# Kernel optimization log

Measured on AMD Instinct MI355X. Metric: run time of the kernel, lower is better.

Reference implementation:

```python
import jax, jax.numpy as jnp
import numpy as np

N = 16384
T = 100          # num_timesteps
THR = 1.0        # spike threshold
TAU = 10.0       # tau_mem
WIDTH = 1.0      # surrogate beta (width_grad)
SCALE = 1.0      # surrogate grad scale (scale_grad)
ALPHA = float(np.exp(-1.0 / TAU))  # membrane decay per step


@jax.custom_vjp
def single_spike(v):
    # SingleSpike: at most one spike per step, heaviside on (v - thr)
    return (v >= THR).astype(v.dtype)

def _ss_fwd(v):
    return single_spike(v), v

def _ss_bwd(v, g):
    # SingleExponential surrogate: scale * exp(-beta * |v - thr|)
    return (g * SCALE * jnp.exp(-WIDTH * jnp.abs(v - THR)),)

single_spike.defvjp(_ss_fwd, _ss_bwd)


def setup_inputs() -> dict:
    key = jax.random.key(0)
    k1, k2 = jax.random.split(key)
    x = jax.random.normal(k1, (N, 2, 4, 4, T), dtype=jnp.float32)
    # SLAYER dense weight: Conv3d kernel [out=1, C=2, H=4, W=4] (no bias)
    W = jax.random.normal(k2, (1, 2, 4, 4), dtype=jnp.float32) * 0.1
    return {"x": x, "W": W}


def reference(x, W):
    # dense projection per timestep: [N,C,H,W,T] x [O,C,H,W] -> [N,O,T]
    weighted = jnp.einsum('nchwt,ochw->not', x, W)
    inp_t = jnp.moveaxis(weighted, -1, 0)  # [T, N, 1]

    def step(v, i):
        # sinabs LIF with norm_input=True: v = alpha*v + (1-alpha)*input
        v = ALPHA * v + (1.0 - ALPHA) * i
        s = single_spike(v)
        return v - s * THR, s  # MembraneSubtract reset

    v0 = jnp.zeros(inp_t.shape[1:], dtype=weighted.dtype)
    _, spikes = jax.lax.scan(step, v0, inp_t)  # spikes: [T, N, 1]
    out = jnp.moveaxis(spikes, 0, -1)          # [N, 1, T]
    return out.reshape(x.shape[0], 1, 1, 1, T)  # match Conv3d output shape
```

## Files before the change

### kernel.cpp

```cpp
#include <hip/hip_runtime.h>


#define T_STEPS 100
#define CHW     32
#define NPB     16
#define PITCH   101

__global__ __launch_bounds__(256, 4)
void exodus_fused(const float* __restrict__ x,
                  const float* __restrict__ W,
                  float* __restrict__ out) {
    __shared__ float s_in[NPB][PITCH];
    __shared__ float s_sp[NPB][PITCH];

    const int tid    = threadIdx.x;
    const int lane   = tid & 63;
    const int wv     = tid >> 6;
    const int n_base = blockIdx.x * NPB;

    float Wr[CHW];
    #pragma unroll
    for (int c = 0; c < CHW; ++c) Wr[c] = W[c];

    if (lane < T_STEPS / 2) {
        for (int i = 0; i < NPB / 4; ++i) {
            const int nl = wv * (NPB / 4) + i;
            const float* xp = x + (size_t)(n_base + nl) * (CHW * T_STEPS) + 2 * lane;
            float a0 = 0.f, a1 = 0.f;
            #pragma unroll
            for (int c = 0; c < CHW; ++c) {
                const float2 v = *reinterpret_cast<const float2*>(xp + c * T_STEPS);
                a0 += Wr[c] * v.x;
                a1 += Wr[c] * v.y;
            }
            s_in[nl][2 * lane]     = a0;
            s_in[nl][2 * lane + 1] = a1;
        }
    }
    __syncthreads();

    if (lane < NPB / 4) {
        const int nl = wv * (NPB / 4) + lane;
        const float A = 0.9048374180359595f;
        const float B = 0.0951625819640404f;
        float v = 0.f;
        #pragma unroll 4
        for (int t = 0; t < T_STEPS; ++t) {
            v = A * v + B * s_in[nl][t];
            const float sp = (v >= 1.0f) ? 1.0f : 0.0f;
            v -= sp;
            s_sp[nl][t] = sp;
        }
    }
    __syncthreads();

    float* op = out + (size_t)n_base * T_STEPS;
    for (int k = tid; k < NPB * T_STEPS; k += 256) {
        op[k] = s_sp[k / T_STEPS][k % T_STEPS];
    }
}

extern "C" void kernel_launch(void* const* d_in, const int* in_sizes, int n_in,
                              void* d_out, int out_size, void* d_ws, size_t ws_size,
                              hipStream_t stream) {
    const float* x = (const float*)d_in[0];
    const float* W = (const float*)d_in[1];
    float* out = (float*)d_out;

    const int N = in_sizes[0] / (CHW * T_STEPS);
    const int grid = N / NPB;
    exodus_fused<<<grid, 256, 0, stream>>>(x, W, out);
}
```

Measured before the change: 38.66 us.

## Halve neurons per block and software-pipeline x loads with double register buffers

```diff
diff --git a/kernel.cpp b/kernel.cpp
--- a/kernel.cpp
+++ b/kernel.cpp
@@ -3,7 +3,8 @@
 
 #define T_STEPS 100
 #define CHW     32
-#define NPB     16
+#define NPW     2
+#define NPB     8
 #define PITCH   101
 
 __global__ __launch_bounds__(256, 4)
@@ -23,30 +24,62 @@
     for (int c = 0; c < CHW; ++c) Wr[c] = W[c];
 
     if (lane < T_STEPS / 2) {
-        for (int i = 0; i < NPB / 4; ++i) {
-            const int nl = wv * (NPB / 4) + i;
-            const float* xp = x + (size_t)(n_base + nl) * (CHW * T_STEPS) + 2 * lane;
-            float a0 = 0.f, a1 = 0.f;
-            #pragma unroll
-            for (int c = 0; c < CHW; ++c) {
-                const float2 v = *reinterpret_cast<const float2*>(xp + c * T_STEPS);
-                a0 += Wr[c] * v.x;
-                a1 += Wr[c] * v.y;
-            }
-            s_in[nl][2 * lane]     = a0;
-            s_in[nl][2 * lane + 1] = a1;
+        const float* xw = x + (size_t)(n_base + wv * NPW) * (CHW * T_STEPS) + 2 * lane;
+        const int NSTR = CHW * T_STEPS;
+
+        float2 bA[16], bB[16];
+        #pragma unroll
+        for (int j = 0; j < 16; ++j)
+            bA[j] = *reinterpret_cast<const float2*>(xw + j * T_STEPS);
+        #pragma unroll
+        for (int j = 0; j < 16; ++j)
+            bB[j] = *reinterpret_cast<const float2*>(xw + (16 + j) * T_STEPS);
+
+        float n0x = 0.f, n0y = 0.f;
+        #pragma unroll
+        for (int j = 0; j < 16; ++j) {
+            n0x = fmaf(Wr[j], bA[j].x, n0x);
+            n0y = fmaf(Wr[j], bA[j].y, n0y);
         }
+        #pragma unroll
+        for (int j = 0; j < 16; ++j)
+            bA[j] = *reinterpret_cast<const float2*>(xw + NSTR + j * T_STEPS);
+        #pragma unroll
+        for (int j = 0; j < 16; ++j) {
+            n0x = fmaf(Wr[16 + j], bB[j].x, n0x);
+            n0y = fmaf(Wr[16 + j], bB[j].y, n0y);
+        }
+        s_in[wv * NPW + 0][2 * lane]     = n0x;
+        s_in[wv * NPW + 0][2 * lane + 1] = n0y;
+
+        #pragma unroll
+        for (int j = 0; j < 16; ++j)
+            bB[j] = *reinterpret_cast<const float2*>(xw + NSTR + (16 + j) * T_STEPS);
+
+        float n1x = 0.f, n1y = 0.f;
+        #pragma unroll
+        for (int j = 0; j < 16; ++j) {
+            n1x = fmaf(Wr[j], bA[j].x, n1x);
+            n1y = fmaf(Wr[j], bA[j].y, n1y);
+        }
+        #pragma unroll
+        for (int j = 0; j < 16; ++j) {
+            n1x = fmaf(Wr[16 + j], bB[j].x, n1x);
+            n1y = fmaf(Wr[16 + j], bB[j].y, n1y);
+        }
+        s_in[wv * NPW + 1][2 * lane]     = n1x;
+        s_in[wv * NPW + 1][2 * lane + 1] = n1y;
     }
     __syncthreads();
 
-    if (lane < NPB / 4) {
-        const int nl = wv * (NPB / 4) + lane;
+    if (lane < NPW) {
+        const int nl = wv * NPW + lane;
         const float A = 0.9048374180359595f;
         const float B = 0.0951625819640404f;
         float v = 0.f;
         #pragma unroll 4
         for (int t = 0; t < T_STEPS; ++t) {
-            v = A * v + B * s_in[nl][t];
+            v = fmaf(A, v, B * s_in[nl][t]);
             const float sp = (v >= 1.0f) ? 1.0f : 0.0f;
             v -= sp;
             s_sp[nl][t] = sp;
```

After: 37.28 us (median of 2 runs). -3.6%, faster.

## Use float4 loads with explicit double-buffering and halve neurons per block

Applied to the files above, without the earlier changes.

```diff
diff --git a/kernel.cpp b/kernel.cpp
--- a/kernel.cpp
+++ b/kernel.cpp
@@ -3,8 +3,9 @@
 
 #define T_STEPS 100
 #define CHW     32
-#define NPB     16
-#define PITCH   101
+#define NPW     2
+#define NPB     8
+#define PITCH   104
 
 __global__ __launch_bounds__(256, 4)
 void exodus_fused(const float* __restrict__ x,
@@ -22,31 +23,69 @@
     #pragma unroll
     for (int c = 0; c < CHW; ++c) Wr[c] = W[c];
 
-    if (lane < T_STEPS / 2) {
-        for (int i = 0; i < NPB / 4; ++i) {
-            const int nl = wv * (NPB / 4) + i;
-            const float* xp = x + (size_t)(n_base + nl) * (CHW * T_STEPS) + 2 * lane;
-            float a0 = 0.f, a1 = 0.f;
-            #pragma unroll
-            for (int c = 0; c < CHW; ++c) {
-                const float2 v = *reinterpret_cast<const float2*>(xp + c * T_STEPS);
-                a0 += Wr[c] * v.x;
-                a1 += Wr[c] * v.y;
-            }
-            s_in[nl][2 * lane]     = a0;
-            s_in[nl][2 * lane + 1] = a1;
+    if (lane < 50) {
+        const int nl = lane / 25;
+        const int qd = lane - nl * 25;
+        const float* xp = x + (size_t)(n_base + wv * NPW + nl) * (CHW * T_STEPS)
+                        + qd * 4;
+
+        float4 bA[8], bB[8];
+        float4 acc = {0.f, 0.f, 0.f, 0.f};
+
+        #pragma unroll
+        for (int j = 0; j < 8; ++j)
+            bA[j] = *reinterpret_cast<const float4*>(xp + j * T_STEPS);
+        #pragma unroll
+        for (int j = 0; j < 8; ++j)
+            bB[j] = *reinterpret_cast<const float4*>(xp + (8 + j) * T_STEPS);
+
+        #pragma unroll
+        for (int j = 0; j < 8; ++j) {
+            acc.x = fmaf(Wr[j], bA[j].x, acc.x);
+            acc.y = fmaf(Wr[j], bA[j].y, acc.y);
+            acc.z = fmaf(Wr[j], bA[j].z, acc.z);
+            acc.w = fmaf(Wr[j], bA[j].w, acc.w);
         }
+        #pragma unroll
+        for (int j = 0; j < 8; ++j)
+            bA[j] = *reinterpret_cast<const float4*>(xp + (16 + j) * T_STEPS);
+        #pragma unroll
+        for (int j = 0; j < 8; ++j) {
+            acc.x = fmaf(Wr[8 + j], bB[j].x, acc.x);
+            acc.y = fmaf(Wr[8 + j], bB[j].y, acc.y);
+            acc.z = fmaf(Wr[8 + j], bB[j].z, acc.z);
+            acc.w = fmaf(Wr[8 + j], bB[j].w, acc.w);
+        }
+        #pragma unroll
+        for (int j = 0; j < 8; ++j)
+            bB[j] = *reinterpret_cast<const float4*>(xp + (24 + j) * T_STEPS);
+        #pragma unroll
+        for (int j = 0; j < 8; ++j) {
+            acc.x = fmaf(Wr[16 + j], bA[j].x, acc.x);
+            acc.y = fmaf(Wr[16 + j], bA[j].y, acc.y);
+            acc.z = fmaf(Wr[16 + j], bA[j].z, acc.z);
+            acc.w = fmaf(Wr[16 + j], bA[j].w, acc.w);
+        }
+        #pragma unroll
+        for (int j = 0; j < 8; ++j) {
+            acc.x = fmaf(Wr[24 + j], bB[j].x, acc.x);
+            acc.y = fmaf(Wr[24 + j], bB[j].y, acc.y);
+            acc.z = fmaf(Wr[24 + j], bB[j].z, acc.z);
+            acc.w = fmaf(Wr[24 + j], bB[j].w, acc.w);
+        }
+
+        *reinterpret_cast<float4*>(&s_in[wv * NPW + nl][qd * 4]) = acc;
     }
     __syncthreads();
 
-    if (lane < NPB / 4) {
-        const int nl = wv * (NPB / 4) + lane;
+    if (lane < NPW) {
+        const int nl = wv * NPW + lane;
         const float A = 0.9048374180359595f;
         const float B = 0.0951625819640404f;
         float v = 0.f;
         #pragma unroll 4
         for (int t = 0; t < T_STEPS; ++t) {
-            v = A * v + B * s_in[nl][t];
+            v = fmaf(A, v, B * s_in[nl][t]);
             const float sp = (v >= 1.0f) ? 1.0f : 0.0f;
             v -= sp;
             s_sp[nl][t] = sp;
@@ -54,9 +93,12 @@
     }
     __syncthreads();
 
-    float* op = out + (size_t)n_base * T_STEPS;
-    for (int k = tid; k < NPB * T_STEPS; k += 256) {
-        op[k] = s_sp[k / T_STEPS][k % T_STEPS];
+    if (tid < NPB * T_STEPS / 4) {
+        const int t4 = tid * 4;
+        const int n  = t4 / T_STEPS;
+        const int t  = t4 - n * T_STEPS;
+        *reinterpret_cast<float4*>(out + (size_t)n_base * T_STEPS + t4) =
+            *reinterpret_cast<const float4*>(&s_sp[n][t]);
     }
 }
 
```

Result: no change. 38.11 us (-1.4%).

## Make each wave independent with register double-buffered loads overlapping the scan

Applied to the files above, without the earlier changes.

```diff
diff --git a/kernel.cpp b/kernel.cpp
--- a/kernel.cpp
+++ b/kernel.cpp
@@ -3,61 +3,104 @@
 
 #define T_STEPS 100
 #define CHW     32
-#define NPB     16
-#define PITCH   101
+#define NPW     2
+#define SLABS   2
+#define PITCH   102
 
 __global__ __launch_bounds__(256, 4)
 void exodus_fused(const float* __restrict__ x,
                   const float* __restrict__ W,
                   float* __restrict__ out) {
-    __shared__ float s_in[NPB][PITCH];
-    __shared__ float s_sp[NPB][PITCH];
+    __shared__ float s_in[4][NPW][PITCH];
+    __shared__ float s_sp[4][NPW * T_STEPS];
 
-    const int tid    = threadIdx.x;
-    const int lane   = tid & 63;
-    const int wv     = tid >> 6;
-    const int n_base = blockIdx.x * NPB;
+    const int tid  = threadIdx.x;
+    const int lane = tid & 63;
+    const int wv   = tid >> 6;
+    const int wave_n0 = (blockIdx.x * 4 + wv) * (NPW * SLABS);
+    const int NSTR = CHW * T_STEPS;
 
     float Wr[CHW];
     #pragma unroll
     for (int c = 0; c < CHW; ++c) Wr[c] = W[c];
 
-    if (lane < T_STEPS / 2) {
-        for (int i = 0; i < NPB / 4; ++i) {
-            const int nl = wv * (NPB / 4) + i;
-            const float* xp = x + (size_t)(n_base + nl) * (CHW * T_STEPS) + 2 * lane;
-            float a0 = 0.f, a1 = 0.f;
-            #pragma unroll
-            for (int c = 0; c < CHW; ++c) {
-                const float2 v = *reinterpret_cast<const float2*>(xp + c * T_STEPS);
-                a0 += Wr[c] * v.x;
-                a1 += Wr[c] * v.y;
-            }
-            s_in[nl][2 * lane]     = a0;
-            s_in[nl][2 * lane + 1] = a1;
-        }
+    const bool ldr = (lane < T_STEPS / 2);
+
+    float2 bA[16], bB[16];
+
+#define ISSUE(buf, n_off, c_off)                                              \
+    if (ldr) {                                                                \
+        const float* xp = x + (size_t)(wave_n0 + (n_off)) * NSTR + 2 * lane;  \
+        _Pragma("unroll")                                                     \
+        for (int j = 0; j < 16; ++j)                                          \
+            buf[j] = *reinterpret_cast<const float2*>(xp + ((c_off) + j) * T_STEPS); \
     }
-    __syncthreads();
 
-    if (lane < NPB / 4) {
-        const int nl = wv * (NPB / 4) + lane;
-        const float A = 0.9048374180359595f;
-        const float B = 0.0951625819640404f;
-        float v = 0.f;
-        #pragma unroll 4
-        for (int t = 0; t < T_STEPS; ++t) {
-            v = A * v + B * s_in[nl][t];
-            const float sp = (v >= 1.0f) ? 1.0f : 0.0f;
-            v -= sp;
-            s_sp[nl][t] = sp;
-        }
+#define CONSUME(buf, c_off, ax, ay)                                           \
+    if (ldr) {                                                                \
+        _Pragma("unroll")                                                     \
+        for (int j = 0; j < 16; ++j) {                                        \
+            ax = fmaf(Wr[(c_off) + j], buf[j].x, ax);                         \
+            ay = fmaf(Wr[(c_off) + j], buf[j].y, ay);                         \
+        }                                                                     \
     }
-    __syncthreads();
 
-    float* op = out + (size_t)n_base * T_STEPS;
-    for (int k = tid; k < NPB * T_STEPS; k += 256) {
-        op[k] = s_sp[k / T_STEPS][k % T_STEPS];
+#define STORE_SIN(nl, ax, ay)                                                 \
+    if (ldr) {                                                                \
+        s_in[wv][nl][2 * lane]     = ax;                                      \
+        s_in[wv][nl][2 * lane + 1] = ay;                                      \
     }
+
+#define SCAN()                                                                \
+    if (lane < NPW) {                                                         \
+        const float* si = &s_in[wv][lane][0];                                 \
+        float*       sp = &s_sp[wv][lane * T_STEPS];                          \
+        const float A = 0.9048374180359595f;           \
+        const float Bc = 0.0951625819640404f;                  \
+        float v = 0.f;                                                        \
+        _Pragma("unroll 4")                                                   \
+        for (int t = 0; t < T_STEPS; ++t) {                                   \
+            v = fmaf(A, v, Bc * si[t]);                                       \
+            const float spk = (v >= 1.0f) ? 1.0f : 0.0f;                      \
+            v -= spk;                                  \
+            sp[t] = spk;                                                      \
+        }                                                                     \
+    }
+
+#define WRITEOUT(n_off)                                                       \
+    if (ldr) {                                                                \
+        const float4 r = *reinterpret_cast<const float4*>(&s_sp[wv][lane * 4]); \
+        *reinterpret_cast<float4*>(                                           \
+            out + (size_t)(wave_n0 + (n_off)) * T_STEPS + lane * 4) = r;      \
+    }
+
+    float n0x, n0y, n1x, n1y;
+
+    ISSUE(bA, 0, 0);  ISSUE(bB, 0, 16);
+    n0x = n0y = 0.f;
+    CONSUME(bA, 0, n0x, n0y);
+    ISSUE(bA, 1, 0);
+    CONSUME(bB, 16, n0x, n0y);  STORE_SIN(0, n0x, n0y);
+    ISSUE(bB, 1, 16);
+    n1x = n1y = 0.f;
+    CONSUME(bA, 0, n1x, n1y);
+    CONSUME(bB, 16, n1x, n1y);  STORE_SIN(1, n1x, n1y);
+
+    ISSUE(bA, 2, 0);  ISSUE(bB, 2, 16);
+    SCAN();
+    WRITEOUT(0);
+
+    n0x = n0y = 0.f;
+    CONSUME(bA, 0, n0x, n0y);
+    ISSUE(bA, 3, 0);
+    CONSUME(bB, 16, n0x, n0y);  STORE_SIN(0, n0x, n0y);
+    ISSUE(bB, 3, 16);
+    n1x = n1y = 0.f;
+    CONSUME(bA, 0, n1x, n1y);
+    CONSUME(bB, 16, n1x, n1y);  STORE_SIN(1, n1x, n1y);
+
+    SCAN();
+    WRITEOUT(NPW);
 }
 
 extern "C" void kernel_launch(void* const* d_in, const int* in_sizes, int n_in,
@@ -68,6 +111,6 @@
     float* out = (float*)d_out;
 
     const int N = in_sizes[0] / (CHW * T_STEPS);
-    const int grid = N / NPB;
+    const int grid = N / (4 * NPW * SLABS);
     exodus_fused<<<grid, 256, 0, stream>>>(x, W, out);
 }
```

New measurement: 40.05 us. 1.04x slower.
